# Optimization experiments

Measured on AMD Instinct MI355X. Metric: run time of the kernel, lower is better.

Reference implementation:

```python
import jax, jax.numpy as jnp
import numpy as np

B, C, H, W = 4, 2048, 32, 32
HID, A, G = 512, 9, 20
SCALE = 32.0
POS_T, NEG_T = 0.7, 0.3
W_CONF, W_REG = 1.0, 5.0
EPS = 1e-8


def _anchor_base():
    # gen_anc_centers + gen_anc_base: centers at (i+0.5); anc_w=scale, anc_h=scale*ratio; clipped to feature-map extent
    scales = jnp.array([2.0, 4.0, 6.0])
    ratios = jnp.array([0.5, 1.0, 1.5])
    aw = jnp.repeat(scales, 3)                       # [A]
    ah = (scales[:, None] * ratios[None, :]).reshape(-1)
    xc = (jnp.arange(W) + 0.5)[None, :, None]        # [1,W,1]
    yc = (jnp.arange(H) + 0.5)[:, None, None]        # [H,1,1]
    x1 = jnp.clip(xc - aw / 2, 0.0, W)
    y1 = jnp.clip(yc - ah / 2, 0.0, H)
    x2 = jnp.clip(xc + aw / 2, 0.0, W)
    y2 = jnp.clip(yc + ah / 2, 0.0, H)
    anc = jnp.stack(jnp.broadcast_arrays(x1, y1, x2, y2), axis=-1)  # [H,W,A,4]
    return anc.reshape(-1, 4)                        # [N,4], N = H*W*A


def _conv(x, w, b):
    y = jax.lax.conv_general_dilated(x, w, (1, 1), 'SAME',
                                     dimension_numbers=('NCHW', 'OIHW', 'NCHW'))
    return y + b[None, :, None, None]


def setup_inputs():
    key = jax.random.key(0)
    ks = jax.random.split(key, 8)
    feature_map = jax.random.normal(ks[0], (B, C, H, W), jnp.float32)
    # valid GT boxes in pixel coords of a 1024x1024 image
    ctr = jax.random.uniform(ks[1], (B, G, 2), minval=0.15, maxval=0.85) * 1024.0
    wh = jax.random.uniform(ks[2], (B, G, 2), minval=0.05, maxval=0.30) * 1024.0
    gt_bboxes = jnp.clip(jnp.concatenate([ctr - wh / 2, ctr + wh / 2], -1), 0.0, 1024.0)
    gt_classes = jax.random.randint(ks[3], (B, G), 1, 21)
    f1 = 1.0 / np.sqrt(C * 9)
    f2 = 1.0 / np.sqrt(HID)
    conv1_w = jax.random.uniform(ks[4], (HID, C, 3, 3), jnp.float32, -f1, f1)
    conv1_b = jnp.zeros((HID,), jnp.float32)
    conf_w = jax.random.uniform(ks[5], (A, HID, 1, 1), jnp.float32, -f2, f2)
    conf_b = jnp.zeros((A,), jnp.float32)
    reg_w = jax.random.uniform(ks[6], (A * 4, HID, 1, 1), jnp.float32, -f2, f2)
    reg_b = jnp.zeros((A * 4,), jnp.float32)
    return {"feature_map": feature_map, "gt_bboxes": gt_bboxes, "gt_classes": gt_classes,
            "conv1_w": conv1_w, "conv1_b": conv1_b, "conf_w": conf_w, "conf_b": conf_b,
            "reg_w": reg_w, "reg_b": reg_b}


def reference(feature_map, gt_bboxes, gt_classes, conv1_w, conv1_b, conf_w, conf_b, reg_w, reg_b):
    # ProposalModule (dropout = eval identity)
    hid = jax.nn.relu(_conv(feature_map, conv1_w, conv1_b))
    conf = _conv(hid, conf_w, conf_b).transpose(0, 2, 3, 1).reshape(B, -1)       # [B,N]
    offs = _conv(hid, reg_w, reg_b).transpose(0, 2, 3, 1).reshape(B, -1, 4)      # [B,N,4]

    anc = _anchor_base()                              # [N,4]
    gt = gt_bboxes / SCALE                            # project_bboxes p2a

    # IoU [B,N,G]
    lt = jnp.maximum(anc[None, :, None, :2], gt[:, None, :, :2])
    rb = jnp.minimum(anc[None, :, None, 2:], gt[:, None, :, 2:])
    inter = jnp.clip(rb - lt, 0.0).prod(-1)
    area_a = (anc[:, 2] - anc[:, 0]) * (anc[:, 3] - anc[:, 1])
    area_g = (gt[..., 2] - gt[..., 0]) * (gt[..., 3] - gt[..., 1])
    iou = inter / (area_a[None, :, None] + area_g[:, None, :] - inter + EPS)

    # positive: IoU > pos_thresh OR best anchor for each GT; negative: max IoU < neg_thresh
    max_per_gt = iou.max(axis=1, keepdims=True)
    pos = ((iou > POS_T) | ((iou == max_per_gt) & (max_per_gt > EPS))).any(-1)    # [B,N]
    max_per_anc = iou.max(-1)
    gi = iou.argmax(-1)                               # assigned GT per anchor
    neg = (max_per_anc < NEG_T) & (~pos)

    assigned = jnp.take_along_axis(gt, jnp.broadcast_to(gi[:, :, None], gi.shape + (4,)), axis=1)

    acx = (anc[:, 0] + anc[:, 2]) / 2; acy = (anc[:, 1] + anc[:, 3]) / 2
    aw_ = anc[:, 2] - anc[:, 0];       ah_ = anc[:, 3] - anc[:, 1]
    gcx = (assigned[..., 0] + assigned[..., 2]) / 2; gcy = (assigned[..., 1] + assigned[..., 3]) / 2
    gw = assigned[..., 2] - assigned[..., 0];        gh = assigned[..., 3] - assigned[..., 1]
    gt_off = jnp.stack([(gcx - acx) / (aw_ + EPS), (gcy - acy) / (ah_ + EPS),
                        jnp.log((gw + EPS) / (aw_ + EPS)), jnp.log((gh + EPS) / (ah_ + EPS))], -1)

    posf = pos.astype(conf.dtype)
    negf = neg.astype(conf.dtype)
    # BCE-with-logits, reduction='sum' / batch_size (pos target 1, neg target 0)
    cls_loss = ((jax.nn.softplus(-conf) * posf).sum() + (jax.nn.softplus(conf) * negf).sum()) / B
    d = offs - gt_off
    sl1 = jnp.where(jnp.abs(d) < 1.0, 0.5 * d * d, jnp.abs(d) - 0.5)
    reg_loss = (sl1 * posf[..., None]).sum() / B
    total = W_CONF * cls_loss + W_REG * reg_loss

    # generate_proposals from positive anchors + predicted offsets (mask instead of gather for jit)
    pcx = acx + offs[..., 0] * aw_; pcy = acy + offs[..., 1] * ah_
    pw = aw_ * jnp.exp(offs[..., 2]); ph = ah_ * jnp.exp(offs[..., 3])
    proposals = jnp.stack([pcx - pw / 2, pcy - ph / 2, pcx + pw / 2, pcy + ph / 2], -1)
    proposals = proposals * posf[..., None]
    return total, proposals, pos
```

## Files before the change

kernel.cpp:

```cpp
#include <hip/hip_runtime.h>


typedef __bf16 bf16x8 __attribute__((ext_vector_type(8)));
typedef float floatx4 __attribute__((ext_vector_type(4)));

#define NB 4
#define NC 2048
#define NH 32
#define NW 32
#define NHID 512
#define NA 9
#define NG 20
#define NANC 9216
#define NM 4096

#define OFF_XH    0ull
#define OFF_WT    18939904ull
#define OFF_WH    37814272ull
#define OFF_HB    37863424ull
#define OFF_HEADS 37863680ull
#define OFF_MAXG  38650112ull
#define OFF_SUMS  38650624ull
#define OFF_CTR   38650752ull
#define OFF_HIDP  38650880ull

#define PREP_TX   4096
#define PREP_W    4096
#define PREP_WH   96
#define PREP_HALO 528
#define PREP_NBLK (PREP_TX + PREP_W + PREP_WH + PREP_HALO + 1)

__device__ __forceinline__ unsigned short f2bf(float f) {
  unsigned int u = __float_as_uint(f);
  u = (u + 0x7fffu + ((u >> 16) & 1u)) >> 16;
  return (unsigned short)u;
}

__device__ __forceinline__ void gload16(const void* g, void* l) {
  __builtin_amdgcn_global_load_lds(
      (const __attribute__((address_space(1))) unsigned int*)g,
      (__attribute__((address_space(3))) unsigned int*)l, 16, 0, 0);
}

__constant__ float c_aw[9] = {2.f,2.f,2.f,4.f,4.f,4.f,6.f,6.f,6.f};
__constant__ float c_ah[9] = {1.f,2.f,3.f,2.f,4.f,6.f,3.f,6.f,9.f};

struct Anc { float x1, y1, x2, y2, areaA; };
__device__ __forceinline__ Anc anc_of(int n) {
  const int a = n % 9, pix = n / 9;
  const int xi = pix & 31, yi = pix >> 5;
  const float hw = c_aw[a]*0.5f, hh = c_ah[a]*0.5f;
  const float xc = xi + 0.5f, yc = yi + 0.5f;
  Anc A;
  A.x1 = fminf(fmaxf(xc - hw, 0.f), 32.f);
  A.y1 = fminf(fmaxf(yc - hh, 0.f), 32.f);
  A.x2 = fminf(fmaxf(xc + hw, 0.f), 32.f);
  A.y2 = fminf(fmaxf(yc + hh, 0.f), 32.f);
  A.areaA = __fmul_rn(__fsub_rn(A.x2, A.x1), __fsub_rn(A.y2, A.y1));
  return A;
}
__device__ __forceinline__ float iou_one(const Anc& A, float4 gp) {
  const float gx1 = gp.x * 0.03125f, gy1 = gp.y * 0.03125f;
  const float gx2 = gp.z * 0.03125f, gy2 = gp.w * 0.03125f;
  const float dx = fmaxf(__fsub_rn(fminf(A.x2, gx2), fmaxf(A.x1, gx1)), 0.f);
  const float dy = fmaxf(__fsub_rn(fminf(A.y2, gy2), fmaxf(A.y1, gy1)), 0.f);
  const float inter = __fmul_rn(dx, dy);
  const float areaG = __fmul_rn(__fsub_rn(gx2, gx1), __fsub_rn(gy2, gy1));
  const float den = __fadd_rn(__fsub_rn(__fadd_rn(A.areaA, areaG), inter), 1e-8f);
  return __fdiv_rn(inter, den);
}

__global__ __launch_bounds__(256) void k_prep(const float* __restrict__ x,
                                              const float* __restrict__ w1,
                                              const float* __restrict__ cw, const float* __restrict__ cb,
                                              const float* __restrict__ rw, const float* __restrict__ rb,
                                              unsigned short* __restrict__ xh,
                                              unsigned short* __restrict__ wt,
                                              unsigned short* __restrict__ wh, float* __restrict__ hb,
                                              unsigned int* __restrict__ maxg,
                                              float* __restrict__ sums, unsigned int* __restrict__ ctr) {
  const int bid = blockIdx.x;
  const int tid = threadIdx.x;

  if (bid < PREP_TX) {
    __shared__ float tile[64][33];
    const int c0 = (bid & 31) << 6;
    const int h  = (bid >> 5) & 31;
    const int b  = bid >> 10;
    const int w = tid & 31, cl = tid >> 5;
    const float* src = x + (((size_t)b*NC + c0)*NH + h)*NW;
#pragma unroll
    for (int j = 0; j < 8; ++j) {
      const int c = cl + j*8;
      tile[c][w] = src[(size_t)c*NH*NW + w];
    }
    __syncthreads();
    unsigned short* dst = xh + ((size_t)(b*34 + h + 1)*34 + 1)*2048 + c0;
    const int c2 = (tid & 31)*2, wr = tid >> 5;
#pragma unroll
    for (int j = 0; j < 4; ++j) {
      const int ww = wr + j*8;
      const unsigned int lo = f2bf(tile[c2][ww]), hi = f2bf(tile[c2+1][ww]);
      *(unsigned int*)(dst + (size_t)ww*2048 + c2) = lo | (hi << 16);
    }
    return;
  }
  if (bid < PREP_TX + PREP_W) {
    const int t = (bid - PREP_TX)*256 + tid;
    const float* src = w1 + (size_t)t * 9;
#pragma unroll
    for (int g = 0; g < 9; ++g)
      wt[(size_t)g*NHID*NC + t] = f2bf(src[g]);
    return;
  }
  if (bid < PREP_TX + PREP_W + PREP_WH) {
    const int t = (bid - PREP_TX - PREP_W)*256 + tid;
    const int n = t >> 9, c = t & 511;
    float v = 0.f;
    if (n < 9) v = cw[n*512 + c];
    else if (n < 45) v = rw[(n-9)*512 + c];
    wh[t] = f2bf(v);
    if (c == 0) {
      float bv = 0.f;
      if (n < 9) bv = cb[n];
      else if (n < 45) bv = rb[n-9];
      hb[n] = bv;
    }
    return;
  }
  if (bid < PREP_TX + PREP_W + PREP_WH + PREP_HALO) {
    const int q = bid - (PREP_TX + PREP_W + PREP_WH);
    const int b = q / 132, hc = q - b*132;
    int hh, ww;
    if (hc < 34)       { hh = 0;        ww = hc; }
    else if (hc < 68)  { hh = 33;       ww = hc - 34; }
    else if (hc < 100) { hh = hc - 67;  ww = 0; }
    else               { hh = hc - 99;  ww = 33; }
    uint4* dst = (uint4*)(xh + ((size_t)((b*34 + hh)*34 + ww))*2048);
    dst[tid] = make_uint4(0u, 0u, 0u, 0u);
    return;
  }
  if (tid < 80) maxg[tid] = 0u;
  else if (tid < 82) sums[tid - 80] = 0.f;
  else if (tid == 82) *ctr = 0u;
}

__global__ __launch_bounds__(256, 4) void k_conv_gemm(const unsigned short* __restrict__ xh,
                                                      const unsigned short* __restrict__ wt,
                                                      unsigned short* __restrict__ hidp, int csplit) {
  __shared__ unsigned short As[128*64] __attribute__((aligned(16)));
  __shared__ unsigned short Bs[128*64] __attribute__((aligned(16)));
  const int t = threadIdx.x;
  const int tileM = blockIdx.x, tileN = blockIdx.y, kz = blockIdx.z;
  const int b = tileM >> 3, h0 = (tileM & 7) << 2;
  const int o0 = tileN << 7;
  const int wv = t >> 6, lane = t & 63;
  const int wm = wv >> 1, wn = wv & 1;
  const int quad = lane >> 4, l16 = lane & 15;
  const int c_base = kz * csplit;

  floatx4 acc[4][4];
#pragma unroll
  for (int mt = 0; mt < 4; ++mt)
#pragma unroll
    for (int nt = 0; nt < 4; ++nt)
      acc[mt][nt] = (floatx4){0.f, 0.f, 0.f, 0.f};

  const int lr = lane >> 3, pos = lane & 7;
  int gA[4], gB[4];
#pragma unroll
  for (int j = 0; j < 4; ++j) {
    const int row = wv*32 + j*8 + lr;
    const int sd = (pos - row) & 7;
    const int hh = h0 + (row >> 5) + 1, ww = (row & 31) + 1;
    gA[j] = ((b*34 + hh)*34 + ww)*2048 + c_base + sd*8;
    gB[j] = (o0 + row)*2048 + c_base + sd*8;
  }

  for (int g = 0; g < 9; ++g) {
    const int dsp = ((g/3 - 1)*34 + (g%3 - 1)) * 2048;
    const unsigned short* wgp = wt + (size_t)g*NHID*NC;
    for (int c0 = 0; c0 < csplit; c0 += 64) {
#pragma unroll
      for (int j = 0; j < 4; ++j) {
        gload16(xh + gA[j] + dsp + c0, As + (wv*32 + j*8)*64);
        gload16(wgp + gB[j] + c0,      Bs + (wv*32 + j*8)*64);
      }
      __syncthreads();
#pragma unroll
      for (int sub = 0; sub < 2; ++sub) {
        const int ps = ((sub*4 + quad) + l16) & 7;
        bf16x8 af[4], bw[4];
#pragma unroll
        for (int mt = 0; mt < 4; ++mt)
          af[mt] = *(const bf16x8*)(As + (wm*64 + mt*16 + l16)*64 + ps*8);
#pragma unroll
        for (int nt = 0; nt < 4; ++nt)
          bw[nt] = *(const bf16x8*)(Bs + (wn*64 + nt*16 + l16)*64 + ps*8);
#pragma unroll
        for (int mt = 0; mt < 4; ++mt)
#pragma unroll
          for (int nt = 0; nt < 4; ++nt)
            acc[mt][nt] = __builtin_amdgcn_mfma_f32_16x16x32_bf16(af[mt], bw[nt], acc[mt][nt], 0, 0, 0);
      }
      __syncthreads();
    }
  }
  unsigned short* hp = hidp + (size_t)kz*NM*NHID;
#pragma unroll
  for (int mt = 0; mt < 4; ++mt) {
    const int m = tileM*128 + wm*64 + mt*16 + quad*4;
#pragma unroll
    for (int nt = 0; nt < 4; ++nt) {
      const int o = o0 + wn*64 + nt*16 + l16;
#pragma unroll
      for (int r = 0; r < 4; ++r)
        hp[(size_t)(m + r)*NHID + o] = f2bf(acc[mt][nt][r]);
    }
  }
}

__global__ __launch_bounds__(256) void k_heads_fused(const unsigned short* __restrict__ hidp,
                                                     const float* __restrict__ b1,
                                                     const unsigned short* __restrict__ wh,
                                                     const float* __restrict__ hb,
                                                     const float* __restrict__ gtb,
                                                     float* __restrict__ heads,
                                                     unsigned int* __restrict__ maxg,
                                                     int nsplit) {
  const int t = threadIdx.x;
  const int bid = blockIdx.x;
  if (bid >= 64) {
    __shared__ float red[4];
    const int p = bid - 64, b = p / NG, g = p - b*NG;
    const float4 gp = *(const float4*)(gtb + ((size_t)b*NG + g)*4);
    float m = 0.f;
#pragma unroll
    for (int j = 0; j < 36; ++j) {
      const Anc A = anc_of(t + j*256);
      m = fmaxf(m, iou_one(A, gp));
    }
#pragma unroll
    for (int o = 32; o > 0; o >>= 1) m = fmaxf(m, __shfl_xor(m, o));
    if ((t & 63) == 0) red[t >> 6] = m;
    __syncthreads();
    if (t == 0) {
      m = fmaxf(fmaxf(red[0], red[1]), fmaxf(red[2], red[3]));
      maxg[b*NG + g] = __float_as_uint(m);
    }
    return;
  }
  __shared__ unsigned short As[64*40] __attribute__((aligned(16)));
  __shared__ unsigned short Bs[48*40] __attribute__((aligned(16)));
  const int tile = bid;
  const int wv = t >> 6, lane = t & 63;
  const int quad = lane >> 4, l16 = lane & 15;
  floatx4 acc[3];
#pragma unroll
  for (int nt = 0; nt < 3; ++nt) acc[nt] = (floatx4){0.f, 0.f, 0.f, 0.f};
  const int row0 = t >> 2, seg = t & 3;
  for (int c0 = 0; c0 < 512; c0 += 32) {
    {
      const size_t gi = ((size_t)(tile*64 + row0))*512 + c0 + seg*8;
      float s[8] = {0.f,0.f,0.f,0.f,0.f,0.f,0.f,0.f};
      for (int sp = 0; sp < nsplit; ++sp) {
        const uint4 v = *(const uint4*)(hidp + (size_t)sp*NM*NHID + gi);
        s[0] += __uint_as_float(v.x << 16); s[1] += __uint_as_float(v.x & 0xffff0000u);
        s[2] += __uint_as_float(v.y << 16); s[3] += __uint_as_float(v.y & 0xffff0000u);
        s[4] += __uint_as_float(v.z << 16); s[5] += __uint_as_float(v.z & 0xffff0000u);
        s[6] += __uint_as_float(v.w << 16); s[7] += __uint_as_float(v.w & 0xffff0000u);
      }
      const int cb0 = c0 + seg*8;
      unsigned int pk[4];
#pragma unroll
      for (int k = 0; k < 4; ++k) {
        const unsigned int lo = f2bf(fmaxf(s[2*k]   + b1[cb0 + 2*k],     0.f));
        const unsigned int hi = f2bf(fmaxf(s[2*k+1] + b1[cb0 + 2*k + 1], 0.f));
        pk[k] = lo | (hi << 16);
      }
      *(uint4*)(As + row0*40 + seg*8) = make_uint4(pk[0], pk[1], pk[2], pk[3]);
    }
    if (t < 192)
      *(uint4*)(Bs + row0*40 + seg*8) =
          *(const uint4*)(wh + (size_t)row0*512 + c0 + seg*8);
    __syncthreads();
    const bf16x8 af = *(const bf16x8*)(As + (wv*16 + l16)*40 + quad*8);
#pragma unroll
    for (int nt = 0; nt < 3; ++nt) {
      const bf16x8 bw = *(const bf16x8*)(Bs + (nt*16 + l16)*40 + quad*8);
      acc[nt] = __builtin_amdgcn_mfma_f32_16x16x32_bf16(af, bw, acc[nt], 0, 0, 0);
    }
    __syncthreads();
  }
  const int m = tile*64 + wv*16 + quad*4;
#pragma unroll
  for (int nt = 0; nt < 3; ++nt) {
    const int nn = nt*16 + l16;
    const float bv = hb[nn];
#pragma unroll
    for (int r = 0; r < 4; ++r)
      heads[(size_t)(m + r)*48 + nn] = acc[nt][r] + bv;
  }
}

__device__ __forceinline__ float softplusf(float z) {
  return fmaxf(z, 0.f) + log1pf(expf(-fabsf(z)));
}
__device__ __forceinline__ float sl1f(float d) {
  const float ad = fabsf(d);
  return ad < 1.f ? 0.5f*d*d : ad - 0.5f;
}

__global__ __launch_bounds__(256) void k_assign(const unsigned int* __restrict__ maxg,
                                                const float* __restrict__ heads,
                                                const float* __restrict__ gtb,
                                                float* __restrict__ out,
                                                float* __restrict__ sums,
                                                unsigned int* __restrict__ ctr) {
  const int idx = blockIdx.x*256 + threadIdx.x;
  const int b = idx / NANC, n = idx - b*NANC;
  const int a = n % 9, pix = n / 9;
  const Anc A = anc_of(n);

  float mx = -1.f; int gi = 0; bool pos = false;
  for (int g = 0; g < NG; ++g) {
    const float4 gp = *(const float4*)(gtb + ((size_t)b*NG + g)*4);
    const float v = iou_one(A, gp);
    const float mg = __uint_as_float(maxg[b*NG + g]);
    pos = pos || (v > 0.7f) || ((v == mg) && (mg > 1e-8f));
    if (v > mx) { mx = v; gi = g; }
  }
  const bool neg = (mx < 0.3f) && !pos;
  const float posf = pos ? 1.f : 0.f;

  const int m = b*1024 + pix;
  const float* hrow = heads + (size_t)m*48;
  const float conf = hrow[a];
  const float of0 = hrow[9 + a*4 + 0];
  const float of1 = hrow[9 + a*4 + 1];
  const float of2 = hrow[9 + a*4 + 2];
  const float of3 = hrow[9 + a*4 + 3];

  float cls = 0.f;
  if (pos) cls = softplusf(-conf);
  else if (neg) cls = softplusf(conf);

  const float acx = (A.x1 + A.x2)*0.5f, acy = (A.y1 + A.y2)*0.5f;
  const float aw = A.x2 - A.x1, ah = A.y2 - A.y1;
  float reg = 0.f;
  if (pos) {
    const float4 gp = *(const float4*)(gtb + ((size_t)b*NG + gi)*4);
    const float gx1 = gp.x*0.03125f, gy1 = gp.y*0.03125f;
    const float gx2 = gp.z*0.03125f, gy2 = gp.w*0.03125f;
    const float gcx = (gx1+gx2)*0.5f, gcy = (gy1+gy2)*0.5f;
    const float gw = gx2-gx1, gh = gy2-gy1;
    const float t0 = (gcx-acx)/(aw+1e-8f), t1 = (gcy-acy)/(ah+1e-8f);
    const float t2 = logf((gw+1e-8f)/(aw+1e-8f)), t3 = logf((gh+1e-8f)/(ah+1e-8f));
    reg = sl1f(of0-t0) + sl1f(of1-t1) + sl1f(of2-t2) + sl1f(of3-t3);
  }

  const float pcx = acx + of0*aw, pcy = acy + of1*ah;
  const float pw = aw*expf(of2), ph = ah*expf(of3);
  float* op = out + 1 + (size_t)idx*4;
  op[0] = (pcx - pw*0.5f)*posf;
  op[1] = (pcy - ph*0.5f)*posf;
  op[2] = (pcx + pw*0.5f)*posf;
  op[3] = (pcy + ph*0.5f)*posf;
  out[1 + 4*(size_t)NB*NANC + idx] = posf;

  float cs = cls, rs = reg;
#pragma unroll
  for (int o = 32; o > 0; o >>= 1) { cs += __shfl_xor(cs, o); rs += __shfl_xor(rs, o); }
  if ((threadIdx.x & 63) == 0) { atomicAdd(&sums[0], cs); atomicAdd(&sums[1], rs); }

  __syncthreads();
  if (threadIdx.x == 0) {
    __threadfence();
    const unsigned int c = atomicAdd(ctr, 1u);
    if (c == 143u) {
      __threadfence();
      const float fcs = atomicAdd(&sums[0], 0.f);
      const float frs = atomicAdd(&sums[1], 0.f);
      out[0] = fcs*0.25f + 5.f*(frs*0.25f);
    }
  }
}

extern "C" void kernel_launch(void* const* d_in, const int* in_sizes, int n_in,
                              void* d_out, int out_size, void* d_ws, size_t ws_size,
                              hipStream_t stream) {
  const float* x   = (const float*)d_in[0];
  const float* gtb = (const float*)d_in[1];
  const float* w1  = (const float*)d_in[3];
  const float* b1  = (const float*)d_in[4];
  const float* cw  = (const float*)d_in[5];
  const float* cb  = (const float*)d_in[6];
  const float* rw  = (const float*)d_in[7];
  const float* rb  = (const float*)d_in[8];
  float* out = (float*)d_out;
  char* ws = (char*)d_ws;

  unsigned short* xh    = (unsigned short*)(ws + OFF_XH);
  unsigned short* wt    = (unsigned short*)(ws + OFF_WT);
  unsigned short* wh    = (unsigned short*)(ws + OFF_WH);
  float*          hb    = (float*)(ws + OFF_HB);
  float*          heads = (float*)(ws + OFF_HEADS);
  unsigned int*   maxg  = (unsigned int*)(ws + OFF_MAXG);
  float*          sums  = (float*)(ws + OFF_SUMS);
  unsigned int*   ctr   = (unsigned int*)(ws + OFF_CTR);
  unsigned short* hidp  = (unsigned short*)(ws + OFF_HIDP);

  int nsplit = 8;
  while (nsplit > 1 && OFF_HIDP + (size_t)nsplit*NM*NHID*2 > ws_size) nsplit >>= 1;
  const int csplit = NC / nsplit;

  k_prep<<<PREP_NBLK, 256, 0, stream>>>(x, w1, cw, cb, rw, rb, xh, wt, wh, hb, maxg, sums, ctr);
  k_conv_gemm<<<dim3(32, 4, nsplit), 256, 0, stream>>>(xh, wt, hidp, csplit);
  k_heads_fused<<<144, 256, 0, stream>>>(hidp, b1, wh, hb, gtb, heads, maxg, nsplit);
  k_assign<<<144, 256, 0, stream>>>(maxg, heads, gtb, out, sums, ctr);
}
```

Baseline: 246.4 us.

## Fuse heads GEMM with anchor assignment, move max-IoU into prep, remap conv grid

The per-GT max-IoU computation moves into the prep kernel. The heads GEMM and the anchor-assignment/loss kernel are merged, so head outputs stay in LDS instead of a global buffer, which removes one launch and a global round trip. The conv GEMM grid becomes 1-D with the K-split index innermost, so blocks sharing an output tile are scheduled next to each other. The bf16 transpose store in prep is widened to 16-byte writes. The fused kernel runs only 64 blocks, which may limit parallelism in the assignment phase.

New measurement: 246.0 us. About the same (-0.1%).

```diff
diff --git a/kernel.cpp b/kernel.cpp
--- a/kernel.cpp
+++ b/kernel.cpp
@@ -18,17 +18,17 @@
 #define OFF_WT    18939904ull
 #define OFF_WH    37814272ull
 #define OFF_HB    37863424ull
-#define OFF_HEADS 37863680ull
-#define OFF_MAXG  38650112ull
-#define OFF_SUMS  38650624ull
-#define OFF_CTR   38650752ull
-#define OFF_HIDP  38650880ull
+#define OFF_MAXG  37863680ull
+#define OFF_SUMS  37864192ull
+#define OFF_CTR   37864320ull
+#define OFF_HIDP  37864448ull
 
 #define PREP_TX   4096
 #define PREP_W    4096
 #define PREP_WH   96
 #define PREP_HALO 528
-#define PREP_NBLK (PREP_TX + PREP_W + PREP_WH + PREP_HALO + 1)
+#define PREP_MAXG 80
+#define PREP_NBLK (PREP_TX + PREP_W + PREP_WH + PREP_HALO + PREP_MAXG + 1)
 
 __device__ __forceinline__ unsigned short f2bf(float f) {
   unsigned int u = __float_as_uint(f);
@@ -74,16 +74,18 @@
                                               const float* __restrict__ w1,
                                               const float* __restrict__ cw, const float* __restrict__ cb,
                                               const float* __restrict__ rw, const float* __restrict__ rb,
+                                              const float* __restrict__ gtb,
                                               unsigned short* __restrict__ xh,
                                               unsigned short* __restrict__ wt,
                                               unsigned short* __restrict__ wh, float* __restrict__ hb,
                                               unsigned int* __restrict__ maxg,
                                               float* __restrict__ sums, unsigned int* __restrict__ ctr) {
+  __shared__ float tile[64][33];
+  __shared__ float red[4];
   const int bid = blockIdx.x;
   const int tid = threadIdx.x;
 
   if (bid < PREP_TX) {
-    __shared__ float tile[64][33];
     const int c0 = (bid & 31) << 6;
     const int h  = (bid >> 5) & 31;
     const int b  = bid >> 10;
@@ -96,13 +98,15 @@
     }
     __syncthreads();
     unsigned short* dst = xh + ((size_t)(b*34 + h + 1)*34 + 1)*2048 + c0;
-    const int c2 = (tid & 31)*2, wr = tid >> 5;
-#pragma unroll
-    for (int j = 0; j < 4; ++j) {
-      const int ww = wr + j*8;
-      const unsigned int lo = f2bf(tile[c2][ww]), hi = f2bf(tile[c2+1][ww]);
-      *(unsigned int*)(dst + (size_t)ww*2048 + c2) = lo | (hi << 16);
-    }
+    const int w2 = tid >> 3, c8 = (tid & 7) << 3;
+    unsigned int pk[4];
+#pragma unroll
+    for (int k = 0; k < 4; ++k) {
+      const unsigned int lo = f2bf(tile[c8 + 2*k][w2]);
+      const unsigned int hi = f2bf(tile[c8 + 2*k + 1][w2]);
+      pk[k] = lo | (hi << 16);
+    }
+    *(uint4*)(dst + (size_t)w2*2048 + c8) = make_uint4(pk[0], pk[1], pk[2], pk[3]);
     return;
   }
   if (bid < PREP_TX + PREP_W) {
@@ -140,18 +144,37 @@
     dst[tid] = make_uint4(0u, 0u, 0u, 0u);
     return;
   }
-  if (tid < 80) maxg[tid] = 0u;
-  else if (tid < 82) sums[tid - 80] = 0.f;
-  else if (tid == 82) *ctr = 0u;
+  if (bid < PREP_TX + PREP_W + PREP_WH + PREP_HALO + PREP_MAXG) {
+    const int p = bid - (PREP_TX + PREP_W + PREP_WH + PREP_HALO);
+    const int b = p / NG, g = p - b*NG;
+    const float4 gp = *(const float4*)(gtb + ((size_t)b*NG + g)*4);
+    float m = 0.f;
+#pragma unroll
+    for (int j = 0; j < 36; ++j)
+      m = fmaxf(m, iou_one(anc_of(tid + j*256), gp));
+#pragma unroll
+    for (int o = 32; o > 0; o >>= 1) m = fmaxf(m, __shfl_xor(m, o));
+    if ((tid & 63) == 0) red[tid >> 6] = m;
+    __syncthreads();
+    if (tid == 0)
+      maxg[b*NG + g] = __float_as_uint(fmaxf(fmaxf(red[0], red[1]), fmaxf(red[2], red[3])));
+    return;
+  }
+  if (tid < 2) sums[tid] = 0.f;
+  else if (tid == 2) *ctr = 0u;
 }
 
 __global__ __launch_bounds__(256, 4) void k_conv_gemm(const unsigned short* __restrict__ xh,
                                                       const unsigned short* __restrict__ wt,
-                                                      unsigned short* __restrict__ hidp, int csplit) {
+                                                      unsigned short* __restrict__ hidp,
+                                                      int csplit, int ksh) {
   __shared__ unsigned short As[128*64] __attribute__((aligned(16)));
   __shared__ unsigned short Bs[128*64] __attribute__((aligned(16)));
   const int t = threadIdx.x;
-  const int tileM = blockIdx.x, tileN = blockIdx.y, kz = blockIdx.z;
+  const int L = blockIdx.x;
+  const int kz = L & ((1 << ksh) - 1);
+  const int rem = L >> ksh;
+  const int tileM = rem & 31, tileN = rem >> 5;
   const int b = tileM >> 3, h0 = (tileM & 7) << 2;
   const int o0 = tileN << 7;
   const int wv = t >> 6, lane = t & 63;
@@ -220,39 +243,38 @@
   }
 }
 
-__global__ __launch_bounds__(256) void k_heads_fused(const unsigned short* __restrict__ hidp,
-                                                     const float* __restrict__ b1,
-                                                     const unsigned short* __restrict__ wh,
-                                                     const float* __restrict__ hb,
-                                                     const float* __restrict__ gtb,
-                                                     float* __restrict__ heads,
-                                                     unsigned int* __restrict__ maxg,
-                                                     int nsplit) {
-  const int t = threadIdx.x;
-  const int bid = blockIdx.x;
-  if (bid >= 64) {
-    __shared__ float red[4];
-    const int p = bid - 64, b = p / NG, g = p - b*NG;
-    const float4 gp = *(const float4*)(gtb + ((size_t)b*NG + g)*4);
-    float m = 0.f;
-#pragma unroll
-    for (int j = 0; j < 36; ++j) {
-      const Anc A = anc_of(t + j*256);
-      m = fmaxf(m, iou_one(A, gp));
-    }
-#pragma unroll
-    for (int o = 32; o > 0; o >>= 1) m = fmaxf(m, __shfl_xor(m, o));
-    if ((t & 63) == 0) red[t >> 6] = m;
-    __syncthreads();
-    if (t == 0) {
-      m = fmaxf(fmaxf(red[0], red[1]), fmaxf(red[2], red[3]));
-      maxg[b*NG + g] = __float_as_uint(m);
-    }
-    return;
-  }
+__device__ __forceinline__ float softplusf(float z) {
+  return fmaxf(z, 0.f) + log1pf(expf(-fabsf(z)));
+}
+__device__ __forceinline__ float sl1f(float d) {
+  const float ad = fabsf(d);
+  return ad < 1.f ? 0.5f*d*d : ad - 0.5f;
+}
+
+__global__ __launch_bounds__(256) void k_heads_assign(const unsigned short* __restrict__ hidp,
+                                                      const float* __restrict__ b1,
+                                                      const unsigned short* __restrict__ wh,
+                                                      const float* __restrict__ hb,
+                                                      const float* __restrict__ gtb,
+                                                      const unsigned int* __restrict__ maxg,
+                                                      float* __restrict__ out,
+                                                      float* __restrict__ sums,
+                                                      unsigned int* __restrict__ ctr,
+                                                      int nsplit) {
   __shared__ unsigned short As[64*40] __attribute__((aligned(16)));
   __shared__ unsigned short Bs[48*40] __attribute__((aligned(16)));
-  const int tile = bid;
+  __shared__ float hl[64][49];
+  __shared__ float4 gt_s[20];
+  __shared__ float  mg_s[20];
+  const int t = threadIdx.x;
+  const int tile = blockIdx.x;
+  const int b = tile >> 4, pix0 = (tile & 15) << 6;
+
+  if (t < 20) {
+    gt_s[t] = *(const float4*)(gtb + ((size_t)b*NG + t)*4);
+    mg_s[t] = __uint_as_float(maxg[b*NG + t]);
+  }
+
   const int wv = t >> 6, lane = t & 63;
   const int quad = lane >> 4, l16 = lane & 15;
   floatx4 acc[3];
@@ -292,92 +314,78 @@
     }
     __syncthreads();
   }
-  const int m = tile*64 + wv*16 + quad*4;
 #pragma unroll
   for (int nt = 0; nt < 3; ++nt) {
     const int nn = nt*16 + l16;
     const float bv = hb[nn];
 #pragma unroll
     for (int r = 0; r < 4; ++r)
-      heads[(size_t)(m + r)*48 + nn] = acc[nt][r] + bv;
-  }
-}
-
-__device__ __forceinline__ float softplusf(float z) {
-  return fmaxf(z, 0.f) + log1pf(expf(-fabsf(z)));
-}
-__device__ __forceinline__ float sl1f(float d) {
-  const float ad = fabsf(d);
-  return ad < 1.f ? 0.5f*d*d : ad - 0.5f;
-}
-
-__global__ __launch_bounds__(256) void k_assign(const unsigned int* __restrict__ maxg,
-                                                const float* __restrict__ heads,
-                                                const float* __restrict__ gtb,
-                                                float* __restrict__ out,
-                                                float* __restrict__ sums,
-                                                unsigned int* __restrict__ ctr) {
-  const int idx = blockIdx.x*256 + threadIdx.x;
-  const int b = idx / NANC, n = idx - b*NANC;
-  const int a = n % 9, pix = n / 9;
-  const Anc A = anc_of(n);
-
-  float mx = -1.f; int gi = 0; bool pos = false;
-  for (int g = 0; g < NG; ++g) {
-    const float4 gp = *(const float4*)(gtb + ((size_t)b*NG + g)*4);
-    const float v = iou_one(A, gp);
-    const float mg = __uint_as_float(maxg[b*NG + g]);
-    pos = pos || (v > 0.7f) || ((v == mg) && (mg > 1e-8f));
-    if (v > mx) { mx = v; gi = g; }
-  }
-  const bool neg = (mx < 0.3f) && !pos;
-  const float posf = pos ? 1.f : 0.f;
-
-  const int m = b*1024 + pix;
-  const float* hrow = heads + (size_t)m*48;
-  const float conf = hrow[a];
-  const float of0 = hrow[9 + a*4 + 0];
-  const float of1 = hrow[9 + a*4 + 1];
-  const float of2 = hrow[9 + a*4 + 2];
-  const float of3 = hrow[9 + a*4 + 3];
-
-  float cls = 0.f;
-  if (pos) cls = softplusf(-conf);
-  else if (neg) cls = softplusf(conf);
-
-  const float acx = (A.x1 + A.x2)*0.5f, acy = (A.y1 + A.y2)*0.5f;
-  const float aw = A.x2 - A.x1, ah = A.y2 - A.y1;
-  float reg = 0.f;
-  if (pos) {
-    const float4 gp = *(const float4*)(gtb + ((size_t)b*NG + gi)*4);
-    const float gx1 = gp.x*0.03125f, gy1 = gp.y*0.03125f;
-    const float gx2 = gp.z*0.03125f, gy2 = gp.w*0.03125f;
-    const float gcx = (gx1+gx2)*0.5f, gcy = (gy1+gy2)*0.5f;
-    const float gw = gx2-gx1, gh = gy2-gy1;
-    const float t0 = (gcx-acx)/(aw+1e-8f), t1 = (gcy-acy)/(ah+1e-8f);
-    const float t2 = logf((gw+1e-8f)/(aw+1e-8f)), t3 = logf((gh+1e-8f)/(ah+1e-8f));
-    reg = sl1f(of0-t0) + sl1f(of1-t1) + sl1f(of2-t2) + sl1f(of3-t3);
-  }
-
-  const float pcx = acx + of0*aw, pcy = acy + of1*ah;
-  const float pw = aw*expf(of2), ph = ah*expf(of3);
-  float* op = out + 1 + (size_t)idx*4;
-  op[0] = (pcx - pw*0.5f)*posf;
-  op[1] = (pcy - ph*0.5f)*posf;
-  op[2] = (pcx + pw*0.5f)*posf;
-  op[3] = (pcy + ph*0.5f)*posf;
-  out[1 + 4*(size_t)NB*NANC + idx] = posf;
-
-  float cs = cls, rs = reg;
+      hl[wv*16 + quad*4 + r][nn] = acc[nt][r] + bv;
+  }
+  __syncthreads();
+
+  float cs = 0.f, rs = 0.f;
+#pragma unroll
+  for (int k = 0; k < 3; ++k) {
+    const int q = t + k*256;
+    if (q < 576) {
+      const int pixL = q / 9, a = q - pixL*9;
+      const int pix = pix0 + pixL;
+      const int n = pix*9 + a;
+      const int idx = b*NANC + n;
+      const Anc A = anc_of(n);
+
+      float mx = -1.f; int gi = 0; bool pos = false;
+      for (int g = 0; g < NG; ++g) {
+        const float v = iou_one(A, gt_s[g]);
+        const float mg = mg_s[g];
+        pos = pos || (v > 0.7f) || ((v == mg) && (mg > 1e-8f));
+        if (v > mx) { mx = v; gi = g; }
+      }
+      const bool neg = (mx < 0.3f) && !pos;
+      const float posf = pos ? 1.f : 0.f;
+
+      const float conf = hl[pixL][a];
+      const float of0 = hl[pixL][9 + a*4 + 0];
+      const float of1 = hl[pixL][9 + a*4 + 1];
+      const float of2 = hl[pixL][9 + a*4 + 2];
+      const float of3 = hl[pixL][9 + a*4 + 3];
+
+      if (pos) cs += softplusf(-conf);
+      else if (neg) cs += softplusf(conf);
+
+      const float acx = (A.x1 + A.x2)*0.5f, acy = (A.y1 + A.y2)*0.5f;
+      const float aw = A.x2 - A.x1, ah = A.y2 - A.y1;
+      if (pos) {
+        const float4 gp = gt_s[gi];
+        const float gx1 = gp.x*0.03125f, gy1 = gp.y*0.03125f;
+        const float gx2 = gp.z*0.03125f, gy2 = gp.w*0.03125f;
+        const float gcx = (gx1+gx2)*0.5f, gcy = (gy1+gy2)*0.5f;
+        const float gw = gx2-gx1, gh = gy2-gy1;
+        const float t0 = (gcx-acx)/(aw+1e-8f), t1 = (gcy-acy)/(ah+1e-8f);
+        const float t2 = logf((gw+1e-8f)/(aw+1e-8f)), t3 = logf((gh+1e-8f)/(ah+1e-8f));
+        rs += sl1f(of0-t0) + sl1f(of1-t1) + sl1f(of2-t2) + sl1f(of3-t3);
+      }
+
+      const float pcx = acx + of0*aw, pcy = acy + of1*ah;
+      const float pw = aw*expf(of2), ph = ah*expf(of3);
+      float* op = out + 1 + (size_t)idx*4;
+      op[0] = (pcx - pw*0.5f)*posf;
+      op[1] = (pcy - ph*0.5f)*posf;
+      op[2] = (pcx + pw*0.5f)*posf;
+      op[3] = (pcy + ph*0.5f)*posf;
+      out[1 + 4*(size_t)NB*NANC + idx] = posf;
+    }
+  }
 #pragma unroll
   for (int o = 32; o > 0; o >>= 1) { cs += __shfl_xor(cs, o); rs += __shfl_xor(rs, o); }
-  if ((threadIdx.x & 63) == 0) { atomicAdd(&sums[0], cs); atomicAdd(&sums[1], rs); }
+  if ((t & 63) == 0) { atomicAdd(&sums[0], cs); atomicAdd(&sums[1], rs); }
 
   __syncthreads();
-  if (threadIdx.x == 0) {
+  if (t == 0) {
     __threadfence();
     const unsigned int c = atomicAdd(ctr, 1u);
-    if (c == 143u) {
+    if (c == 63u) {
       __threadfence();
       const float fcs = atomicAdd(&sums[0], 0.f);
       const float frs = atomicAdd(&sums[1], 0.f);
@@ -404,18 +412,16 @@
   unsigned short* wt    = (unsigned short*)(ws + OFF_WT);
   unsigned short* wh    = (unsigned short*)(ws + OFF_WH);
   float*          hb    = (float*)(ws + OFF_HB);
-  float*          heads = (float*)(ws + OFF_HEADS);
   unsigned int*   maxg  = (unsigned int*)(ws + OFF_MAXG);
   float*          sums  = (float*)(ws + OFF_SUMS);
   unsigned int*   ctr   = (unsigned int*)(ws + OFF_CTR);
   unsigned short* hidp  = (unsigned short*)(ws + OFF_HIDP);
 
-  int nsplit = 8;
-  while (nsplit > 1 && OFF_HIDP + (size_t)nsplit*NM*NHID*2 > ws_size) nsplit >>= 1;
+  int nsplit = 8, ksh = 3;
+  while (nsplit > 1 && OFF_HIDP + (size_t)nsplit*NM*NHID*2 > ws_size) { nsplit >>= 1; --ksh; }
   const int csplit = NC / nsplit;
 
-  k_prep<<<PREP_NBLK, 256, 0, stream>>>(x, w1, cw, cb, rw, rb, xh, wt, wh, hb, maxg, sums, ctr);
-  k_conv_gemm<<<dim3(32, 4, nsplit), 256, 0, stream>>>(xh, wt, hidp, csplit);
-  k_heads_fused<<<144, 256, 0, stream>>>(hidp, b1, wh, hb, gtb, heads, maxg, nsplit);
-  k_assign<<<144, 256, 0, stream>>>(maxg, heads, gtb, out, sums, ctr);
-}
+  k_prep<<<PREP_NBLK, 256, 0, stream>>>(x, w1, cw, cb, rw, rb, gtb, xh, wt, wh, hb, maxg, sums, ctr);
+  k_conv_gemm<<<128*nsplit, 256, 0, stream>>>(xh, wt, hidp, csplit, ksh);
+  k_heads_assign<<<64, 256, 0, stream>>>(hidp, b1, wh, hb, gtb, maxg, out, sums, ctr, nsplit);
+}
```
